# Kernel optimization log

Hardware: AMD Instinct MI355X
Metric: run time of the kernel (lower is better)

Reference implementation:

```python
import jax, jax.numpy as jnp
import numpy as np

N_NODES = 100000


def gcn_conv(x, edge_index, edge_weight, W, b):
    """PyG GCNConv: out = D^-1/2 (A + I) D^-1/2 X W + b (self-loop weight 1)."""
    n = x.shape[0]
    src, dst = edge_index[0], edge_index[1]
    loop = jnp.arange(n)
    src_sl = jnp.concatenate([src, loop])
    dst_sl = jnp.concatenate([dst, loop])
    ew_sl = jnp.concatenate([edge_weight, jnp.ones((n,), x.dtype)])
    deg = jax.ops.segment_sum(ew_sl, dst_sl, num_segments=n)  # [N]
    dinv = jnp.where(deg > 0, jax.lax.rsqrt(deg), 0.0)
    norm = dinv[src_sl] * ew_sl * dinv[dst_sl]  # [E+N]
    h = x @ W  # [N, out_dim] dense transform before propagation
    msg = h[src_sl] * norm[:, None]  # gather + scale, [E+N, out_dim]
    out = jax.ops.segment_sum(msg, dst_sl, num_segments=n)  # scatter-add
    return out + b


def setup_inputs() -> dict:
    key = jax.random.key(0)
    ks = jax.random.split(key, 9)
    in_dim, hidden, latent = 128, 64, 32
    n, e = N_NODES, 1600000
    x = jax.random.normal(ks[0], (n, in_dim), dtype=jnp.float32)
    edge_index = jax.random.randint(ks[1], (2, e), 0, n, dtype=jnp.int64)
    edge_weight = jax.random.uniform(ks[2], (e,), dtype=jnp.float32)
    def glorot(k, fan_in, fan_out):
        s = jnp.sqrt(6.0 / (fan_in + fan_out))
        return jax.random.uniform(k, (fan_in, fan_out), jnp.float32, -s, s)
    return {
        "x": x,
        "edge_index": edge_index,
        "edge_weight": edge_weight,
        "W1": glorot(ks[3], in_dim, hidden),
        "b1": jnp.zeros((hidden,), jnp.float32),
        "W_mu": glorot(ks[4], hidden, latent),
        "b_mu": jnp.zeros((latent,), jnp.float32),
        "W_lv": glorot(ks[5], hidden, latent),
        "b_lv": jnp.zeros((latent,), jnp.float32),
    }


def reference(x, edge_index, edge_weight, W1, b1, W_mu, b_mu, W_lv, b_lv):
    h = jax.nn.relu(gcn_conv(x, edge_index, edge_weight, W1, b1))
    mu = gcn_conv(h, edge_index, edge_weight, W_mu, b_mu)
    logvar = gcn_conv(h, edge_index, edge_weight, W_lv, b_lv)
    return (mu, logvar)
```

## Files before the change

### kernel.cpp

```cpp
#include <hip/hip_runtime.h>

static __device__ __forceinline__ float4 ld4(const float* p) { return *(const float4*)p; }
static __device__ __forceinline__ float b2f(unsigned short u) {
    return __uint_as_float((unsigned)u << 16);
}
static __device__ __forceinline__ float b2f_lo(unsigned u) { return __uint_as_float(u << 16); }
static __device__ __forceinline__ float b2f_hi(unsigned u) { return __uint_as_float(u & 0xFFFF0000u); }
static __device__ __forceinline__ unsigned short f2b(float f) {
    unsigned x = __float_as_uint(f);
    return (unsigned short)((x + 0x7FFFu + ((x >> 16) & 1u)) >> 16);
}

#define NPB 256
#define CAPE 5120


__global__ __launch_bounds__(256) void k_fused1(const float* __restrict__ A,
                                                const float* __restrict__ W0,
                                                const float* __restrict__ dinv_unused,
                                                unsigned short* __restrict__ gout,
                                                const int* __restrict__ src,
                                                const int* __restrict__ dst,
                                                const float* __restrict__ ew,
                                                int* __restrict__ bin_cnt,
                                                unsigned long long* __restrict__ ebuf,
                                                int n, int E, int gb, int NB) {
    __shared__ float Ws[64 * 64];
    __shared__ float Xs[64 * 64];
    __shared__ int hist[512];
    __shared__ int hbase[512];
    int tid = threadIdx.x;

    if ((int)blockIdx.x < gb) {
        int row0 = blockIdx.x * 64;
        int c0 = (tid & 15) * 4;
        int r0 = (tid >> 4) * 4;
        float4 acc[4] = {};
        #pragma unroll
        for (int p = 0; p < 2; p++) {
            for (int j = tid; j < 1024; j += 256)
                *(float4*)&Ws[j * 4] = ld4(W0 + p * 4096 + j * 4);
            for (int j = tid; j < 1024; j += 256) {
                int r = j >> 4, kc = j & 15;
                int grow = row0 + r;
                float4 v = make_float4(0.f, 0.f, 0.f, 0.f);
                if (grow < n) v = ld4(A + (size_t)grow * 128 + p * 64 + kc * 4);
                *(float4*)&Xs[r * 64 + kc * 4] = v;
            }
            __syncthreads();
            #pragma unroll 4
            for (int kk = 0; kk < 64; kk += 4) {
                float4 w0 = ld4(&Ws[(kk + 0) * 64 + c0]);
                float4 w1 = ld4(&Ws[(kk + 1) * 64 + c0]);
                float4 w2 = ld4(&Ws[(kk + 2) * 64 + c0]);
                float4 w3 = ld4(&Ws[(kk + 3) * 64 + c0]);
                #pragma unroll
                for (int i = 0; i < 4; i++) {
                    float4 a = ld4(&Xs[(r0 + i) * 64 + kk]);
                    acc[i].x = fmaf(a.x, w0.x, fmaf(a.y, w1.x, fmaf(a.z, w2.x, fmaf(a.w, w3.x, acc[i].x))));
                    acc[i].y = fmaf(a.x, w0.y, fmaf(a.y, w1.y, fmaf(a.z, w2.y, fmaf(a.w, w3.y, acc[i].y))));
                    acc[i].z = fmaf(a.x, w0.z, fmaf(a.y, w1.z, fmaf(a.z, w2.z, fmaf(a.w, w3.z, acc[i].z))));
                    acc[i].w = fmaf(a.x, w0.w, fmaf(a.y, w1.w, fmaf(a.z, w2.w, fmaf(a.w, w3.w, acc[i].w))));
                }
            }
            __syncthreads();
        }
        #pragma unroll
        for (int i = 0; i < 4; i++) {
            int grow = row0 + r0 + i;
            if (grow < n) {
                ushort4 u = make_ushort4(f2b(acc[i].x), f2b(acc[i].y), f2b(acc[i].z), f2b(acc[i].w));
                *(ushort4*)&gout[(size_t)grow * 64 + c0] = u;
            }
        }
    } else {
        for (int j = tid; j < NB; j += 256) hist[j] = 0;
        __syncthreads();
        int e0 = ((int)blockIdx.x - gb) * 4096;
        unsigned long long pk[16]; int bb[16]; int loc[16];
        #pragma unroll
        for (int j = 0; j < 16; j++) {
            int e = e0 + j * 256 + tid;
            if (e < E) {
                int s = src[e];
                int d = dst[e];
                float w = ew[e];
                bb[j] = d >> 8;
                pk[j] = ((unsigned long long)__float_as_uint(w) << 32) |
                        (unsigned)((d & (NPB - 1)) << 17) | (unsigned)s;
                loc[j] = atomicAdd(&hist[bb[j]], 1);
            } else bb[j] = -1;
        }
        __syncthreads();
        for (int j = tid; j < NB; j += 256) hbase[j] = atomicAdd(&bin_cnt[j], hist[j]);
        __syncthreads();
        #pragma unroll
        for (int j = 0; j < 16; j++) {
            if (bb[j] >= 0)
                ebuf[(size_t)bb[j] * CAPE + hbase[bb[j]] + loc[j]] = pk[j];
        }
    }
}

__global__ __launch_bounds__(512) void k_csr_build(const unsigned long long* __restrict__ ebuf,
                                                   const int* __restrict__ bin_cnt,
                                                   int2* __restrict__ rowcnt,
                                                   float* __restrict__ dinv,
                                                   unsigned long long* __restrict__ csr,
                                                   int n) {
    __shared__ unsigned long long eL[CAPE];
    __shared__ unsigned cntL[NPB];
    __shared__ unsigned ewsL[NPB];
    __shared__ unsigned fillL[NPB];
    __shared__ int scanL[512];
    __shared__ int rowL[NPB];
    __shared__ int binbase_s;
    int b = blockIdx.x;
    int tid = threadIdx.x;
    if (tid < NPB) { cntL[tid] = 0; ewsL[tid] = 0; fillL[tid] = 0; }
    scanL[tid] = (tid < b) ? bin_cnt[tid] : 0;
    __syncthreads();
    int m = bin_cnt[b];
    const unsigned long long* eb = ebuf + (size_t)b * CAPE;
    for (int i = tid; i < m; i += 512) {
        unsigned long long pk = eb[i];
        eL[i] = pk;
        int ld = (int)((pk >> 17) & (NPB - 1));
        float w = __uint_as_float((unsigned)(pk >> 32));
        atomicAdd(&cntL[ld], 1u);
        atomicAdd(&ewsL[ld], (unsigned)(w * 16777216.0f));
    }
    __syncthreads();
    #pragma unroll
    for (int off = 256; off > 0; off >>= 1) {
        if (tid < off) scanL[tid] += scanL[tid + off];
        __syncthreads();
    }
    if (tid == 0) binbase_s = scanL[0];
    __syncthreads();
    int v = (tid < NPB) ? (int)cntL[tid] : 0;
    scanL[tid] = v;
    __syncthreads();
    #pragma unroll
    for (int off = 1; off < 512; off <<= 1) {
        int t = (tid >= off) ? scanL[tid - off] : 0;
        __syncthreads();
        scanL[tid] += t;
        __syncthreads();
    }
    if (tid < NPB) {
        int rp = binbase_s + scanL[tid] - v;
        rowL[tid] = rp;
        int node = b * NPB + tid;
        if (node < n) {
            rowcnt[node] = make_int2(rp, v);
            dinv[node] = rsqrtf(1.0f + (float)ewsL[tid] * (1.0f / 16777216.0f));
        }
    }
    __syncthreads();
    for (int i = tid; i < m; i += 512) {
        unsigned long long pk = eL[i];
        int s = (int)(pk & 0x1FFFF);
        int ld = (int)((pk >> 17) & (NPB - 1));
        int pos = rowL[ld] + (int)atomicAdd(&fillL[ld], 1u);
        csr[pos] = (unsigned long long)(unsigned)s | (pk & 0xFFFFFFFF00000000ull);
    }
}

__global__ __launch_bounds__(256) void k_scale(unsigned short* __restrict__ h0,
                                               const float* __restrict__ dinv, int n) {
    int i = blockIdx.x * 256 + threadIdx.x;
    if (i >= n * 16) return;
    int node = i >> 4;
    float sc = dinv[node];
    ushort4 u = *(ushort4*)&h0[(size_t)i * 4];
    u = make_ushort4(f2b(b2f(u.x) * sc), f2b(b2f(u.y) * sc),
                     f2b(b2f(u.z) * sc), f2b(b2f(u.w) * sc));
    *(ushort4*)&h0[(size_t)i * 4] = u;
}

template<int K, bool SPLITW, bool ABF16>
__global__ __launch_bounds__(256) void k_gemm(const void* __restrict__ Av,
                                              const float* __restrict__ W0,
                                              const float* __restrict__ W1s,
                                              const float* __restrict__ dinv,
                                              unsigned short* __restrict__ out, int n) {
    __shared__ float Ws[K * 64];
    __shared__ float Xs[64 * K];
    int tid = threadIdx.x;
    int row0 = blockIdx.x * 64;

    constexpr int WF4 = K * 64 / 4;
    for (int j = tid; j < WF4; j += 256) {
        float4 v;
        if (!SPLITW) {
            v = ld4(W0 + j * 4);
        } else {
            int k = (j * 4) >> 6;
            int c = (j * 4) & 63;
            v = (c < 32) ? ld4(W0 + k * 32 + c) : ld4(W1s + k * 32 + (c - 32));
        }
        *(float4*)&Ws[j * 4] = v;
    }
    constexpr int XF4PR = K / 4;
    for (int j = tid; j < 64 * XF4PR; j += 256) {
        int r = j / XF4PR, kc = j % XF4PR;
        int grow = row0 + r;
        float4 v = make_float4(0.f, 0.f, 0.f, 0.f);
        if (grow < n) {
            if (ABF16) {
                const unsigned short* Ab = (const unsigned short*)Av;
                ushort4 u = *(const ushort4*)(Ab + (size_t)grow * K + kc * 4);
                v = make_float4(b2f(u.x), b2f(u.y), b2f(u.z), b2f(u.w));
            } else {
                v = ld4((const float*)Av + (size_t)grow * K + kc * 4);
            }
        }
        *(float4*)&Xs[r * K + kc * 4] = v;
    }
    __syncthreads();

    int c0 = (tid & 15) * 4;
    int r0 = (tid >> 4) * 4;
    float4 acc[4] = {};
    #pragma unroll 4
    for (int kk = 0; kk < K; kk += 4) {
        float4 w0 = ld4(&Ws[(kk + 0) * 64 + c0]);
        float4 w1 = ld4(&Ws[(kk + 1) * 64 + c0]);
        float4 w2 = ld4(&Ws[(kk + 2) * 64 + c0]);
        float4 w3 = ld4(&Ws[(kk + 3) * 64 + c0]);
        #pragma unroll
        for (int i = 0; i < 4; i++) {
            float4 a = ld4(&Xs[(r0 + i) * K + kk]);
            acc[i].x = fmaf(a.x, w0.x, fmaf(a.y, w1.x, fmaf(a.z, w2.x, fmaf(a.w, w3.x, acc[i].x))));
            acc[i].y = fmaf(a.x, w0.y, fmaf(a.y, w1.y, fmaf(a.z, w2.y, fmaf(a.w, w3.y, acc[i].y))));
            acc[i].z = fmaf(a.x, w0.z, fmaf(a.y, w1.z, fmaf(a.z, w2.z, fmaf(a.w, w3.z, acc[i].z))));
            acc[i].w = fmaf(a.x, w0.w, fmaf(a.y, w1.w, fmaf(a.z, w2.w, fmaf(a.w, w3.w, acc[i].w))));
        }
    }
    #pragma unroll
    for (int i = 0; i < 4; i++) {
        int grow = row0 + r0 + i;
        if (grow < n) {
            float sc = dinv[grow];
            ushort4 u = make_ushort4(f2b(acc[i].x * sc), f2b(acc[i].y * sc),
                                     f2b(acc[i].z * sc), f2b(acc[i].w * sc));
            *(ushort4*)&out[(size_t)grow * 64 + c0] = u;
        }
    }
}

template<bool RELU, bool SPLIT_OUT>
__global__ __launch_bounds__(256) void k_prop(const unsigned short* __restrict__ g,
                                              const int2* __restrict__ csr,
                                              const int2* __restrict__ rowcnt,
                                              const float* __restrict__ dinv,
                                              const float* __restrict__ bias0,
                                              const float* __restrict__ bias1,
                                              void* __restrict__ outv, int n) {
    int node = blockIdx.x * 4 + (threadIdx.x >> 6);
    if (node >= n) return;
    int lane = threadIdx.x & 63;
    int q = lane >> 4;
    int t = lane & 15;
    float a0 = 0.f, a1 = 0.f, a2 = 0.f, a3 = 0.f;
    int2 rc = rowcnt[node];
    const int2* ep = csr + rc.x;
    int m = rc.y;
    for (int e = 0; e < m; e += 8) {
        int e1 = e + q, e2 = e + 4 + q;
        if (e1 < m) {
            int2 p = ep[e1];
            uint2 r = *(const uint2*)(g + (size_t)p.x * 64 + t * 4);
            float nm = __int_as_float(p.y);
            a0 = fmaf(b2f_lo(r.x), nm, a0);
            a1 = fmaf(b2f_hi(r.x), nm, a1);
            a2 = fmaf(b2f_lo(r.y), nm, a2);
            a3 = fmaf(b2f_hi(r.y), nm, a3);
        }
        if (e2 < m) {
            int2 p = ep[e2];
            uint2 r = *(const uint2*)(g + (size_t)p.x * 64 + t * 4);
            float nm = __int_as_float(p.y);
            a0 = fmaf(b2f_lo(r.x), nm, a0);
            a1 = fmaf(b2f_hi(r.x), nm, a1);
            a2 = fmaf(b2f_lo(r.y), nm, a2);
            a3 = fmaf(b2f_hi(r.y), nm, a3);
        }
    }
    a0 += __shfl_xor(a0, 16); a0 += __shfl_xor(a0, 32);
    a1 += __shfl_xor(a1, 16); a1 += __shfl_xor(a1, 32);
    a2 += __shfl_xor(a2, 16); a2 += __shfl_xor(a2, 32);
    a3 += __shfl_xor(a3, 16); a3 += __shfl_xor(a3, 32);
    if (q != 0) return;
    uint2 sr = *(const uint2*)(g + (size_t)node * 64 + t * 4);
    a0 += b2f_lo(sr.x); a1 += b2f_hi(sr.x);
    a2 += b2f_lo(sr.y); a3 += b2f_hi(sr.y);
    float di = dinv[node];
    a0 *= di; a1 *= di; a2 *= di; a3 *= di;
    if (!SPLIT_OUT) {
        float4 bb = ld4(bias0 + t * 4);
        a0 += bb.x; a1 += bb.y; a2 += bb.z; a3 += bb.w;
        if (RELU) {
            a0 = fmaxf(a0, 0.f); a1 = fmaxf(a1, 0.f);
            a2 = fmaxf(a2, 0.f); a3 = fmaxf(a3, 0.f);
        }
        ushort4 u = make_ushort4(f2b(a0), f2b(a1), f2b(a2), f2b(a3));
        *(ushort4*)((unsigned short*)outv + (size_t)node * 64 + t * 4) = u;
    } else {
        float* out = (float*)outv;
        if (t < 8) {
            float4 bb = ld4(bias0 + t * 4);
            float4 v = make_float4(a0 + bb.x, a1 + bb.y, a2 + bb.z, a3 + bb.w);
            *(float4*)&out[(size_t)node * 32 + t * 4] = v;
        } else {
            float4 bb = ld4(bias1 + (t - 8) * 4);
            float4 v = make_float4(a0 + bb.x, a1 + bb.y, a2 + bb.z, a3 + bb.w);
            *(float4*)&out[(size_t)n * 32 + (size_t)node * 32 + (t - 8) * 4] = v;
        }
    }
}

extern "C" void kernel_launch(void* const* d_in, const int* in_sizes, int n_in,
                              void* d_out, int out_size, void* d_ws, size_t ws_size,
                              hipStream_t stream) {
    const float* x   = (const float*)d_in[0];
    const int*   ei  = (const int*)d_in[1];
    const float* ew  = (const float*)d_in[2];
    const float* W1  = (const float*)d_in[3];
    const float* b1  = (const float*)d_in[4];
    const float* Wmu = (const float*)d_in[5];
    const float* bmu = (const float*)d_in[6];
    const float* Wlv = (const float*)d_in[7];
    const float* blv = (const float*)d_in[8];
    float* outp = (float*)d_out;

    const int n = in_sizes[0] / 128;
    const int E = in_sizes[2];
    const int* src = ei;
    const int* dst = ei + E;
    const int NB = (n + NPB - 1) / NPB;

    size_t o = 0;
    auto alloc = [&](size_t bytes) { void* p = (char*)d_ws + o; o += (bytes + 511) & ~(size_t)511; return p; };
    int*   bin_cnt  = (int*)alloc((size_t)NB * 4);
    int2*  rowcnt   = (int2*)alloc((size_t)n * 8);
    float* dinv     = (float*)alloc((size_t)n * 4);
    unsigned long long* csr  = (unsigned long long*)alloc((size_t)E * 8);
    unsigned long long* ebuf = (unsigned long long*)alloc((size_t)NB * CAPE * 8);
    unsigned short* g0 = (unsigned short*)alloc((size_t)n * 64 * 2);
    unsigned short* h  = (unsigned short*)alloc((size_t)n * 64 * 2);
    unsigned short* g2 = g0;

    const int gb = (n + 63) / 64;
    const int bb = (E + 4095) / 4096;

    hipMemsetAsync(bin_cnt, 0, (size_t)NB * 4, stream);
    k_fused1<<<gb + bb, 256, 0, stream>>>(x, W1, nullptr, g0, src, dst, ew,
                                          bin_cnt, ebuf, n, E, gb, NB);
    k_csr_build<<<NB, 512, 0, stream>>>(ebuf, bin_cnt, rowcnt, dinv, csr, n);
    k_scale<<<(n * 16 + 255) / 256, 256, 0, stream>>>(g0, dinv, n);
    k_prop<true, false><<<(n + 3) / 4, 256, 0, stream>>>(g0, (const int2*)csr, rowcnt, dinv,
                                                         b1, nullptr, h, n);
    k_gemm<64, true, true><<<gb, 256, 0, stream>>>(h, Wmu, Wlv, dinv, g2, n);
    k_prop<false, true><<<(n + 3) / 4, 256, 0, stream>>>(g2, (const int2*)csr, rowcnt, dinv,
                                                         bmu, blv, outp, n);
}
```

Measured before the change: 319.0 us.

## Reorder second GCN layer to aggregate first, then fuse GEMM into propagation

The second layer now aggregates the pre-scaled hidden features and then applies the mu/logvar weight matrices inside the same kernel, using associativity (A·H)·W. Layer 1's propagation applies bias, ReLU and the next layer's dinv source scaling directly, so the separate GEMM kernel and its intermediate write/read go away. The risk is the fused kernel's per-block structure: each wave serially processes 16 nodes with larger shared memory (about 33KB), which may lower occupancy and latency hiding for the gather phase.

```diff
diff --git a/kernel.cpp b/kernel.cpp
--- a/kernel.cpp
+++ b/kernel.cpp
@@ -17,8 +17,7 @@
 
 __global__ __launch_bounds__(256) void k_fused1(const float* __restrict__ A,
                                                 const float* __restrict__ W0,
-                                                const float* __restrict__ dinv_unused,
-                                                unsigned short* __restrict__ gout,
+                                                unsigned short* __restrict__ hout,
                                                 const int* __restrict__ src,
                                                 const int* __restrict__ dst,
                                                 const float* __restrict__ ew,
@@ -70,7 +69,7 @@
             int grow = row0 + r0 + i;
             if (grow < n) {
                 ushort4 u = make_ushort4(f2b(acc[i].x), f2b(acc[i].y), f2b(acc[i].z), f2b(acc[i].w));
-                *(ushort4*)&gout[(size_t)grow * 64 + c0] = u;
+                *(ushort4*)&hout[(size_t)grow * 64 + c0] = u;
             }
         }
     } else {
@@ -179,85 +178,12 @@
     *(ushort4*)&h0[(size_t)i * 4] = u;
 }
 
-template<int K, bool SPLITW, bool ABF16>
-__global__ __launch_bounds__(256) void k_gemm(const void* __restrict__ Av,
-                                              const float* __restrict__ W0,
-                                              const float* __restrict__ W1s,
-                                              const float* __restrict__ dinv,
-                                              unsigned short* __restrict__ out, int n) {
-    __shared__ float Ws[K * 64];
-    __shared__ float Xs[64 * K];
-    int tid = threadIdx.x;
-    int row0 = blockIdx.x * 64;
-
-    constexpr int WF4 = K * 64 / 4;
-    for (int j = tid; j < WF4; j += 256) {
-        float4 v;
-        if (!SPLITW) {
-            v = ld4(W0 + j * 4);
-        } else {
-            int k = (j * 4) >> 6;
-            int c = (j * 4) & 63;
-            v = (c < 32) ? ld4(W0 + k * 32 + c) : ld4(W1s + k * 32 + (c - 32));
-        }
-        *(float4*)&Ws[j * 4] = v;
-    }
-    constexpr int XF4PR = K / 4;
-    for (int j = tid; j < 64 * XF4PR; j += 256) {
-        int r = j / XF4PR, kc = j % XF4PR;
-        int grow = row0 + r;
-        float4 v = make_float4(0.f, 0.f, 0.f, 0.f);
-        if (grow < n) {
-            if (ABF16) {
-                const unsigned short* Ab = (const unsigned short*)Av;
-                ushort4 u = *(const ushort4*)(Ab + (size_t)grow * K + kc * 4);
-                v = make_float4(b2f(u.x), b2f(u.y), b2f(u.z), b2f(u.w));
-            } else {
-                v = ld4((const float*)Av + (size_t)grow * K + kc * 4);
-            }
-        }
-        *(float4*)&Xs[r * K + kc * 4] = v;
-    }
-    __syncthreads();
-
-    int c0 = (tid & 15) * 4;
-    int r0 = (tid >> 4) * 4;
-    float4 acc[4] = {};
-    #pragma unroll 4
-    for (int kk = 0; kk < K; kk += 4) {
-        float4 w0 = ld4(&Ws[(kk + 0) * 64 + c0]);
-        float4 w1 = ld4(&Ws[(kk + 1) * 64 + c0]);
-        float4 w2 = ld4(&Ws[(kk + 2) * 64 + c0]);
-        float4 w3 = ld4(&Ws[(kk + 3) * 64 + c0]);
-        #pragma unroll
-        for (int i = 0; i < 4; i++) {
-            float4 a = ld4(&Xs[(r0 + i) * K + kk]);
-            acc[i].x = fmaf(a.x, w0.x, fmaf(a.y, w1.x, fmaf(a.z, w2.x, fmaf(a.w, w3.x, acc[i].x))));
-            acc[i].y = fmaf(a.x, w0.y, fmaf(a.y, w1.y, fmaf(a.z, w2.y, fmaf(a.w, w3.y, acc[i].y))));
-            acc[i].z = fmaf(a.x, w0.z, fmaf(a.y, w1.z, fmaf(a.z, w2.z, fmaf(a.w, w3.z, acc[i].z))));
-            acc[i].w = fmaf(a.x, w0.w, fmaf(a.y, w1.w, fmaf(a.z, w2.w, fmaf(a.w, w3.w, acc[i].w))));
-        }
-    }
-    #pragma unroll
-    for (int i = 0; i < 4; i++) {
-        int grow = row0 + r0 + i;
-        if (grow < n) {
-            float sc = dinv[grow];
-            ushort4 u = make_ushort4(f2b(acc[i].x * sc), f2b(acc[i].y * sc),
-                                     f2b(acc[i].z * sc), f2b(acc[i].w * sc));
-            *(ushort4*)&out[(size_t)grow * 64 + c0] = u;
-        }
-    }
-}
-
-template<bool RELU, bool SPLIT_OUT>
-__global__ __launch_bounds__(256) void k_prop(const unsigned short* __restrict__ g,
-                                              const int2* __restrict__ csr,
-                                              const int2* __restrict__ rowcnt,
-                                              const float* __restrict__ dinv,
-                                              const float* __restrict__ bias0,
-                                              const float* __restrict__ bias1,
-                                              void* __restrict__ outv, int n) {
+__global__ __launch_bounds__(256) void k_prop1(const unsigned short* __restrict__ g,
+                                               const int2* __restrict__ csr,
+                                               const int2* __restrict__ rowcnt,
+                                               const float* __restrict__ dinv,
+                                               const float* __restrict__ bias0,
+                                               unsigned short* __restrict__ outq, int n) {
     int node = blockIdx.x * 4 + (threadIdx.x >> 6);
     if (node >= n) return;
     int lane = threadIdx.x & 63;
@@ -297,26 +223,108 @@
     a0 += b2f_lo(sr.x); a1 += b2f_hi(sr.x);
     a2 += b2f_lo(sr.y); a3 += b2f_hi(sr.y);
     float di = dinv[node];
-    a0 *= di; a1 *= di; a2 *= di; a3 *= di;
-    if (!SPLIT_OUT) {
-        float4 bb = ld4(bias0 + t * 4);
-        a0 += bb.x; a1 += bb.y; a2 += bb.z; a3 += bb.w;
-        if (RELU) {
-            a0 = fmaxf(a0, 0.f); a1 = fmaxf(a1, 0.f);
-            a2 = fmaxf(a2, 0.f); a3 = fmaxf(a3, 0.f);
-        }
-        ushort4 u = make_ushort4(f2b(a0), f2b(a1), f2b(a2), f2b(a3));
-        *(ushort4*)((unsigned short*)outv + (size_t)node * 64 + t * 4) = u;
-    } else {
-        float* out = (float*)outv;
-        if (t < 8) {
-            float4 bb = ld4(bias0 + t * 4);
-            float4 v = make_float4(a0 + bb.x, a1 + bb.y, a2 + bb.z, a3 + bb.w);
-            *(float4*)&out[(size_t)node * 32 + t * 4] = v;
-        } else {
-            float4 bb = ld4(bias1 + (t - 8) * 4);
-            float4 v = make_float4(a0 + bb.x, a1 + bb.y, a2 + bb.z, a3 + bb.w);
-            *(float4*)&out[(size_t)n * 32 + (size_t)node * 32 + (t - 8) * 4] = v;
+    float4 bb = ld4(bias0 + t * 4);
+    a0 = fmaxf(fmaf(a0, di, bb.x), 0.f) * di;
+    a1 = fmaxf(fmaf(a1, di, bb.y), 0.f) * di;
+    a2 = fmaxf(fmaf(a2, di, bb.z), 0.f) * di;
+    a3 = fmaxf(fmaf(a3, di, bb.w), 0.f) * di;
+    ushort4 u = make_ushort4(f2b(a0), f2b(a1), f2b(a2), f2b(a3));
+    *(ushort4*)(outq + (size_t)node * 64 + t * 4) = u;
+}
+
+__global__ __launch_bounds__(256) void k_prop2g(const unsigned short* __restrict__ qv,
+                                                const int2* __restrict__ csr,
+                                                const int2* __restrict__ rowcnt,
+                                                const float* __restrict__ dinv,
+                                                const float* __restrict__ Wmu,
+                                                const float* __restrict__ Wlv,
+                                                const float* __restrict__ bmu,
+                                                const float* __restrict__ blv,
+                                                float* __restrict__ outp, int n) {
+    __shared__ float accL[64 * 68];
+    __shared__ float Ws[64 * 64];
+    int tid = threadIdx.x;
+    for (int j = tid; j < 1024; j += 256) {
+        int k = (j * 4) >> 6;
+        int c = (j * 4) & 63;
+        float4 v = (c < 32) ? ld4(Wmu + k * 32 + c) : ld4(Wlv + k * 32 + (c - 32));
+        *(float4*)&Ws[j * 4] = v;
+    }
+    int wv = tid >> 6, lane = tid & 63;
+    int q = lane >> 4, t = lane & 15;
+    int node0 = blockIdx.x * 64;
+    for (int i = 0; i < 16; i++) {
+        int node = node0 + wv * 16 + i;
+        float a0 = 0.f, a1 = 0.f, a2 = 0.f, a3 = 0.f;
+        if (node < n) {
+            int2 rc = rowcnt[node];
+            const int2* ep = csr + rc.x;
+            int m = rc.y;
+            for (int e = 0; e < m; e += 8) {
+                int e1 = e + q, e2 = e + 4 + q;
+                if (e1 < m) {
+                    int2 p = ep[e1];
+                    uint2 r = *(const uint2*)(qv + (size_t)p.x * 64 + t * 4);
+                    float nm = __int_as_float(p.y);
+                    a0 = fmaf(b2f_lo(r.x), nm, a0);
+                    a1 = fmaf(b2f_hi(r.x), nm, a1);
+                    a2 = fmaf(b2f_lo(r.y), nm, a2);
+                    a3 = fmaf(b2f_hi(r.y), nm, a3);
+                }
+                if (e2 < m) {
+                    int2 p = ep[e2];
+                    uint2 r = *(const uint2*)(qv + (size_t)p.x * 64 + t * 4);
+                    float nm = __int_as_float(p.y);
+                    a0 = fmaf(b2f_lo(r.x), nm, a0);
+                    a1 = fmaf(b2f_hi(r.x), nm, a1);
+                    a2 = fmaf(b2f_lo(r.y), nm, a2);
+                    a3 = fmaf(b2f_hi(r.y), nm, a3);
+                }
+            }
+            if (q == 0) {
+                uint2 sr = *(const uint2*)(qv + (size_t)node * 64 + t * 4);
+                a0 += b2f_lo(sr.x); a1 += b2f_hi(sr.x);
+                a2 += b2f_lo(sr.y); a3 += b2f_hi(sr.y);
+            }
+        }
+        a0 += __shfl_xor(a0, 16); a0 += __shfl_xor(a0, 32);
+        a1 += __shfl_xor(a1, 16); a1 += __shfl_xor(a1, 32);
+        a2 += __shfl_xor(a2, 16); a2 += __shfl_xor(a2, 32);
+        a3 += __shfl_xor(a3, 16); a3 += __shfl_xor(a3, 32);
+        if (q == 0) {
+            float di = (node < n) ? dinv[node] : 0.f;
+            float4 v = make_float4(a0 * di, a1 * di, a2 * di, a3 * di);
+            *(float4*)&accL[(wv * 16 + i) * 68 + t * 4] = v;
+        }
+    }
+    __syncthreads();
+    int c0 = (tid & 15) * 4;
+    int r0 = (tid >> 4) * 4;
+    float4 acc[4] = {};
+    #pragma unroll 4
+    for (int kk = 0; kk < 64; kk += 4) {
+        float4 w0 = ld4(&Ws[(kk + 0) * 64 + c0]);
+        float4 w1 = ld4(&Ws[(kk + 1) * 64 + c0]);
+        float4 w2 = ld4(&Ws[(kk + 2) * 64 + c0]);
+        float4 w3 = ld4(&Ws[(kk + 3) * 64 + c0]);
+        #pragma unroll
+        for (int i = 0; i < 4; i++) {
+            float4 a = ld4(&accL[(r0 + i) * 68 + kk]);
+            acc[i].x = fmaf(a.x, w0.x, fmaf(a.y, w1.x, fmaf(a.z, w2.x, fmaf(a.w, w3.x, acc[i].x))));
+            acc[i].y = fmaf(a.x, w0.y, fmaf(a.y, w1.y, fmaf(a.z, w2.y, fmaf(a.w, w3.y, acc[i].y))));
+            acc[i].z = fmaf(a.x, w0.z, fmaf(a.y, w1.z, fmaf(a.z, w2.z, fmaf(a.w, w3.z, acc[i].z))));
+            acc[i].w = fmaf(a.x, w0.w, fmaf(a.y, w1.w, fmaf(a.z, w2.w, fmaf(a.w, w3.w, acc[i].w))));
+        }
+    }
+    float4 bb = (c0 < 32) ? ld4(bmu + c0) : ld4(blv + c0 - 32);
+    #pragma unroll
+    for (int i = 0; i < 4; i++) {
+        int row = node0 + r0 + i;
+        if (row < n) {
+            float4 v = make_float4(acc[i].x + bb.x, acc[i].y + bb.y,
+                                   acc[i].z + bb.z, acc[i].w + bb.w);
+            if (c0 < 32) *(float4*)&outp[(size_t)row * 32 + c0] = v;
+            else         *(float4*)&outp[(size_t)n * 32 + (size_t)row * 32 + (c0 - 32)] = v;
         }
     }
 }
@@ -349,20 +357,16 @@
     unsigned long long* csr  = (unsigned long long*)alloc((size_t)E * 8);
     unsigned long long* ebuf = (unsigned long long*)alloc((size_t)NB * CAPE * 8);
     unsigned short* g0 = (unsigned short*)alloc((size_t)n * 64 * 2);
-    unsigned short* h  = (unsigned short*)alloc((size_t)n * 64 * 2);
-    unsigned short* g2 = g0;
+    unsigned short* qb = (unsigned short*)alloc((size_t)n * 64 * 2);
 
     const int gb = (n + 63) / 64;
     const int bb = (E + 4095) / 4096;
 
     hipMemsetAsync(bin_cnt, 0, (size_t)NB * 4, stream);
-    k_fused1<<<gb + bb, 256, 0, stream>>>(x, W1, nullptr, g0, src, dst, ew,
-                                          bin_cnt, ebuf, n, E, gb, NB);
+    k_fused1<<<gb + bb, 256, 0, stream>>>(x, W1, g0, src, dst, ew, bin_cnt, ebuf, n, E, gb, NB);
     k_csr_build<<<NB, 512, 0, stream>>>(ebuf, bin_cnt, rowcnt, dinv, csr, n);
     k_scale<<<(n * 16 + 255) / 256, 256, 0, stream>>>(g0, dinv, n);
-    k_prop<true, false><<<(n + 3) / 4, 256, 0, stream>>>(g0, (const int2*)csr, rowcnt, dinv,
-                                                         b1, nullptr, h, n);
-    k_gemm<64, true, true><<<gb, 256, 0, stream>>>(h, Wmu, Wlv, dinv, g2, n);
-    k_prop<false, true><<<(n + 3) / 4, 256, 0, stream>>>(g2, (const int2*)csr, rowcnt, dinv,
-                                                         bmu, blv, outp, n);
-}
+    k_prop1<<<(n + 3) / 4, 256, 0, stream>>>(g0, (const int2*)csr, rowcnt, dinv, b1, qb, n);
+    k_prop2g<<<gb, 256, 0, stream>>>(qb, (const int2*)csr, rowcnt, dinv,
+                                     Wmu, Wlv, bmu, blv, outp, n);
+}
```

Measured after the change: 373.3 us. +17.0%, slower.
